# Kernel tuning notes

Measured on AMD Instinct MI355X. Metric: run time of the kernel, lower is better.

Reference implementation:

```python
import jax, jax.numpy as jnp
import numpy as np
from jax import lax

B = 512
THRESHOLD = 0.5
CFG = [64, 64, 'M', 128, 128, 'M', 256, 256, 256, 'M', 512, 512, 512, 'M', 512, 512, 512, 'M']  # VGG16


def _conv_relu(x, w, b):
    # x: [B,C,H,W], w: [O,I,3,3] (torch OIHW layout), pad=1 stride=1
    y = lax.conv_general_dilated(x, w, (1, 1), 'SAME',
                                 dimension_numbers=('NCHW', 'OIHW', 'NCHW'))
    return jax.nn.relu(y + b[None, :, None, None])


def _maxpool2(x):
    return lax.reduce_window(x, -jnp.inf, lax.max, (1, 1, 2, 2), (1, 1, 2, 2), 'VALID')


def _features(x, ws, bs):
    i = 0
    for c in CFG:
        if c == 'M':
            x = _maxpool2(x)
        else:
            x = _conv_relu(x, ws[i], bs[i])
            i += 1
    return x  # [B,512,1,1]


def _gcn(distance):
    # Faithful translation, including the source bug: 'onetensor' is zeros_like,
    # so mask==0 everywhere and A_hat collapses to the identity.
    n = distance.shape[0]
    zero = jnp.zeros_like(distance)
    one = jnp.zeros_like(distance)  # bug in original: torch.zeros_like for onetensor
    adj = jnp.where(distance > THRESHOLD, distance, zero)
    mask = jnp.where(distance > THRESHOLD, one, zero)
    idx = lax.top_k(adj, 10)[1]                                   # [n,10]
    top10 = jnp.zeros_like(adj).at[jnp.arange(n)[:, None], idx].set(1.0)
    top10 = top10 * mask
    a_hat = top10 + jnp.eye(n, dtype=distance.dtype)
    d_inv = jnp.diag(1.0 / jnp.sum(a_hat, axis=1))
    return lax.stop_gradient(a_hat @ d_inv)                        # [n,n]


def _forward(x, target, conv_ws, conv_bs, lin1_w, lin1_b, lin2_w, lin2_b, cls_w, cls_b):
    feat = _features(x, conv_ws, conv_bs).reshape(x.shape[0], -1)  # [B,512]
    h = jax.nn.relu(feat @ lin1_w + lin1_b)                        # [B,256]
    low = h @ lin2_w + lin2_b                                      # [B,128]
    graph_pre = jax.nn.sigmoid(low @ low.T)                        # [B,B]
    graph_gt = (target[:, None] == target[None, :]).astype(jnp.float32)
    mat = _gcn(graph_pre)                                          # [B,B], detached
    out = (mat @ feat) @ cls_w + cls_b                             # [B,10]
    return out, graph_pre, graph_gt


def setup_inputs() -> dict:
    key = jax.random.key(0)
    ks = iter(jax.random.split(key, 64))
    inp = {}
    inp['x'] = jax.random.normal(next(ks), (B, 3, 32, 32), dtype=jnp.float32)
    inp['target'] = jax.random.randint(next(ks), (B,), 0, 10)
    in_c, i = 3, 0
    for c in CFG:
        if c == 'M':
            continue
        scale = 1.0 / np.sqrt(in_c * 9.0)
        inp['conv%d_w' % i] = jax.random.normal(next(ks), (c, in_c, 3, 3), dtype=jnp.float32) * scale
        inp['conv%d_b' % i] = jnp.zeros((c,), dtype=jnp.float32)
        in_c, i = c, i + 1
    inp['lin1_w'] = jax.random.normal(next(ks), (512, 256), dtype=jnp.float32) * (1.0 / np.sqrt(512.0))
    inp['lin1_b'] = jnp.zeros((256,), dtype=jnp.float32)
    inp['lin2_w'] = jax.random.normal(next(ks), (256, 128), dtype=jnp.float32) * (1.0 / np.sqrt(256.0))
    inp['lin2_b'] = jnp.zeros((128,), dtype=jnp.float32)
    inp['cls_w'] = jax.random.normal(next(ks), (512, 10), dtype=jnp.float32) * (1.0 / np.sqrt(512.0))
    inp['cls_b'] = jnp.zeros((10,), dtype=jnp.float32)
    return inp


def reference(x, target,
              conv0_w, conv0_b, conv1_w, conv1_b, conv2_w, conv2_b, conv3_w, conv3_b,
              conv4_w, conv4_b, conv5_w, conv5_b, conv6_w, conv6_b, conv7_w, conv7_b,
              conv8_w, conv8_b, conv9_w, conv9_b, conv10_w, conv10_b, conv11_w, conv11_b,
              conv12_w, conv12_b,
              lin1_w, lin1_b, lin2_w, lin2_b, cls_w, cls_b):
    ws = [conv0_w, conv1_w, conv2_w, conv3_w, conv4_w, conv5_w, conv6_w,
          conv7_w, conv8_w, conv9_w, conv10_w, conv11_w, conv12_w]
    bs = [conv0_b, conv1_b, conv2_b, conv3_b, conv4_b, conv5_b, conv6_b,
          conv7_b, conv8_b, conv9_b, conv10_b, conv11_b, conv12_b]
    return _forward(x, target, ws, bs, lin1_w, lin1_b, lin2_w, lin2_b, cls_w, cls_b)
```

## Files before the change

kernel.cpp:

```cpp
#include <hip/hip_runtime.h>

typedef unsigned short u16;
typedef __bf16 bf16x8 __attribute__((ext_vector_type(8)));
typedef float floatx4 __attribute__((ext_vector_type(4)));

__device__ inline u16 f2bf(float f) {
    return __builtin_bit_cast(u16, (__bf16)f);
}
__device__ inline float bf2f(u16 h) {
    return __uint_as_float(((unsigned int)h) << 16);
}

__device__ __forceinline__ void async_copy16(u16* lds, const u16* g) {
    __builtin_amdgcn_global_load_lds(
        (const __attribute__((address_space(1))) unsigned int*)(uintptr_t)g,
        (__attribute__((address_space(3))) unsigned int*)(unsigned int)(uintptr_t)lds,
        16, 0, 0);
}

__global__ void zero_halo(u16* __restrict__ buf, int Hp, int C, int total8)
{
    int i = blockIdx.x * 256 + threadIdx.x;
    if (i >= total8) return;
    int c8 = i % (C / 8);
    int p  = i / (C / 8);
    int ring = 4 * Hp - 4;
    int h = p % ring;
    int b = p / ring;
    int y, x;
    if (h < Hp)              { y = 0;              x = h; }
    else if (h < 2 * Hp)     { y = Hp - 1;         x = h - Hp; }
    else if (h < 3 * Hp - 2) { y = h - 2 * Hp + 1; x = 0; }
    else                     { y = h - 3 * Hp + 3; x = Hp - 1; }
    uint4 z = make_uint4(0u, 0u, 0u, 0u);
    *(uint4*)(buf + ((size_t)((b * Hp + y) * Hp + x) * C) + c8 * 8) = z;
}

__global__ __launch_bounds__(256) void conv0_kernel(
    const float* __restrict__ x, const float* __restrict__ w,
    const float* __restrict__ bias, u16* __restrict__ out)
{
    __shared__ __align__(16) float xs[3][6][36];
    const int t  = threadIdx.x;
    const int b  = blockIdx.x >> 3;
    const int y0 = (blockIdx.x & 7) * 4;

    for (int i = t; i < 3 * 6 * 36; i += 256) {
        int ci  = i / 216;
        int rem = i % 216;
        int r   = rem / 36;
        int c   = rem % 36;
        int gy  = y0 - 1 + r;
        int gx  = c - 1;
        float v = 0.f;
        if ((unsigned)gy < 32u && (unsigned)gx < 32u)
            v = x[((b * 3 + ci) * 32 + gy) * 32 + gx];
        xs[ci][r][c] = v;
    }
    const int lane = t & 63;
    const int wv   = t >> 6;
    float wr[27];
    #pragma unroll
    for (int k = 0; k < 27; k++) wr[k] = w[lane * 27 + k];
    const float bz = bias[lane];
    __syncthreads();

    const int y = y0 + wv;
    u16* orow = out + ((size_t)((b * 34 + y + 1) * 34 + 1) * 64) + lane;
    for (int xg = 0; xg < 32; xg += 4) {
        float a0 = bz, a1 = bz, a2 = bz, a3 = bz;
        #pragma unroll
        for (int ci = 0; ci < 3; ci++) {
            #pragma unroll
            for (int rr = 0; rr < 3; rr++) {
                const float* row = &xs[ci][wv + rr][0];
                float4 c03 = *(const float4*)(row + xg);
                float2 c45 = *(const float2*)(row + xg + 4);
                float w0 = wr[ci * 9 + rr * 3 + 0];
                float w1 = wr[ci * 9 + rr * 3 + 1];
                float w2 = wr[ci * 9 + rr * 3 + 2];
                a0 += c03.x * w0 + c03.y * w1 + c03.z * w2;
                a1 += c03.y * w0 + c03.z * w1 + c03.w * w2;
                a2 += c03.z * w0 + c03.w * w1 + c45.x * w2;
                a3 += c03.w * w0 + c45.x * w1 + c45.y * w2;
            }
        }
        orow[(xg + 0) * 64] = f2bf(fmaxf(a0, 0.f));
        orow[(xg + 1) * 64] = f2bf(fmaxf(a1, 0.f));
        orow[(xg + 2) * 64] = f2bf(fmaxf(a2, 0.f));
        orow[(xg + 3) * 64] = f2bf(fmaxf(a3, 0.f));
    }
}

struct RepackArgs {
    const float* src[14];
    u16* dst[14];
    int p1[14];
    int p2[14];
    int startBlk[15];
    int nseg;
};

__global__ __launch_bounds__(256) void repack_all(RepackArgs a)
{
    __shared__ __align__(16) u16 lds[9216];
    int blk = blockIdx.x;
    int s = 0;
    #pragma unroll 1
    while (s + 1 < a.nseg && blk >= a.startBlk[s + 1]) s++;
    const int cb = blk - a.startBlk[s];
    const int t  = threadIdx.x;

    if (a.p2[s] == 0) {
        const int Cin = a.p1[s];
        const int logCin = __builtin_ctz(Cin);
        const float* src = a.src[s] + (size_t)cb * 9216;
        u16* dst = a.dst[s] + (size_t)cb * 9216;
        #pragma unroll
        for (int it = 0; it < 9; it++) {
            int j4 = it * 256 + t;
            float4 v = *(const float4*)(src + j4 * 4);
            ushort4 h;
            h.x = f2bf(v.x); h.y = f2bf(v.y); h.z = f2bf(v.z); h.w = f2bf(v.w);
            *(ushort4*)(lds + j4 * 4) = h;
        }
        __syncthreads();
        #pragma unroll
        for (int it = 0; it < 9; it++) {
            int o4   = (it * 256 + t) * 4;
            int ci   = o4 & (Cin - 1);
            int rest = o4 >> logCin;
            int co   = rest / 9;
            int sh   = rest - co * 9;
            int sb   = (co << logCin) * 9 + ci * 9 + sh;
            ushort4 h;
            h.x = lds[sb]; h.y = lds[sb + 9]; h.z = lds[sb + 18]; h.w = lds[sb + 27];
            *(ushort4*)(dst + o4) = h;
        }
    } else {
        const int K = a.p1[s], N = a.p2[s];
        const int ntx = N >> 6;
        const int k0 = (cb / ntx) * 64, n0 = (cb % ntx) * 64;
        const float* src = a.src[s];
        u16* dst = a.dst[s];
        const int r = t >> 4, c4 = (t & 15) * 4;
        #pragma unroll
        for (int rr = 0; rr < 64; rr += 16) {
            float4 v = *(const float4*)(src + (size_t)(k0 + r + rr) * N + n0 + c4);
            u16* p = lds + (r + rr) * 72 + c4;
            p[0] = f2bf(v.x); p[1] = f2bf(v.y); p[2] = f2bf(v.z); p[3] = f2bf(v.w);
        }
        __syncthreads();
        #pragma unroll
        for (int it = 0; it < 2; it++) {
            int ov = it * 256 + t;
            int n  = ov >> 3;
            int kq = (ov & 7) * 8;
            __align__(16) u16 h[8];
            #pragma unroll
            for (int j = 0; j < 8; j++) h[j] = lds[(kq + j) * 72 + n];
            *(uint4*)(dst + (size_t)(n0 + n) * K + k0 + kq) = *(uint4*)h;
        }
    }
}

template <int BM, int BN>
__global__ __launch_bounds__(256) void conv_gemm(
    const u16* __restrict__ in, const u16* __restrict__ wt,
    const float* __restrict__ bias, u16* __restrict__ out,
    float* __restrict__ partial, size_t pstride,
    int H, int Cin, int Cout, int logHW, int logW, int splitN,
    int outPad, int poolMode)
{
    constexpr int BK = 64;
    constexpr int WC = (BM == 256) ? BN : (BN / 2);
    constexpr int NT = WC / 16;
    constexpr int NB_A = BM / 32;
    constexpr int NB_B = BN / 32;
    constexpr int ASZ = BM * BK;
    constexpr int BSZ = BN * BK;
    __shared__ u16 As[2 * ASZ];
    __shared__ u16 Bs[2 * BSZ];

    const int Nblocks = Cout / BN;
    const int per = gridDim.x >> 3;
    const int bid = (blockIdx.x & 7) * per + (blockIdx.x >> 3);
    const int sp   = bid % splitN;
    const int tile = bid / splitN;
    const int m0 = (tile / Nblocks) * BM;
    const int n0 = (tile % Nblocks) * BN;

    const int t    = threadIdx.x;
    const int lane = t & 63;
    const int wave = t >> 6;
    const int quad = lane >> 4;
    const int l16  = lane & 15;
    const int wm   = (BM == 256) ? wave : (wave >> 1);
    const int wn   = (BM == 256) ? 0 : (wave & 1);
    const int W    = H;
    const int Wp   = H + 2;
    const int HW   = 1 << logHW;
    const int col8 = t & 7;
    const int r0   = t >> 3;
    const int scol = col8 ^ (r0 & 7);

    const int CinB = Cin * 2;

    int vA[NB_A];
    #pragma unroll
    for (int j = 0; j < NB_A; j++) {
        int m  = m0 + r0 + 32 * j;
        int b  = m >> logHW;
        int rm = m & (HW - 1);
        int y  = rm >> logW;
        int xx = rm & (W - 1);
        vA[j] = ((b * Wp + y + 1) * Wp + xx + 1) * CinB + scol * 16;
    }
    int vB[NB_B];
    #pragma unroll
    for (int j = 0; j < NB_B; j++)
        vB[j] = (n0 + r0 + 32 * j) * 9 * CinB + scol * 16;

    const int logKB = (Cin == 64) ? 0 : (Cin == 128) ? 1 : (Cin == 256) ? 2 : 3;
    const int KB  = 1 << logKB;
    const int T   = 9 * KB;
    const int len = T / splitN;
    const int it0 = sp * len;

    int s0 = it0 >> logKB;
    int c3 = s0 - (s0 / 3) * 3;
    int ta = ((s0 / 3 - 1) * Wp + (c3 - 1)) * CinB;
    int kb = (it0 & (KB - 1)) * 128;
    int tb = it0 * 128;

    const char* const inB = (const char*)in;
    const char* const wtB = (const char*)wt;

    floatx4 acc[4][NT];
    #pragma unroll
    for (int i = 0; i < 4; i++)
        #pragma unroll
        for (int j = 0; j < NT; j++)
            acc[i][j] = (floatx4){0.f, 0.f, 0.f, 0.f};

    const int sw = (l16 & 7) * 8;

    auto stage = [&](int ua, int tbv, int buf) {
        u16* la = As + buf * ASZ + t * 8;
        u16* lb = Bs + buf * BSZ + t * 8;
        #pragma unroll
        for (int j = 0; j < NB_A; j++)
            async_copy16(la + j * 2048, (const u16*)(inB + (ua + vA[j])));
        #pragma unroll
        for (int j = 0; j < NB_B; j++)
            async_copy16(lb + j * 2048, (const u16*)(wtB + (tbv + vB[j])));
    };
    auto advance = [&]() {
        tb += 128;
        kb += 128;
        if (kb == CinB) {
            kb = 0;
            ta += (c3 == 2) ? (Wp - 2) * CinB : CinB;
            c3 = (c3 == 2) ? 0 : c3 + 1;
        }
    };

    stage(ta + kb, tb, 0);
    advance();
    __syncthreads();

    int cur = 0;
    for (int it = 0; it < len; it++) {
        if (it + 1 < len) {
            stage(ta + kb, tb, cur ^ 1);
            advance();
        }
        const u16* Ab = As + cur * ASZ;
        const u16* Bb = Bs + cur * BSZ;
        #pragma unroll
        for (int kk = 0; kk < BK; kk += 32) {
            bf16x8 af[4], bfv[NT];
            int cbo = kk + quad * 8;
            #pragma unroll
            for (int mt = 0; mt < 4; mt++)
                af[mt] = *(const bf16x8*)(Ab + (wm * 64 + mt * 16 + l16) * 64 + (cbo ^ sw));
            #pragma unroll
            for (int nt = 0; nt < NT; nt++)
                bfv[nt] = *(const bf16x8*)(Bb + (wn * WC + nt * 16 + l16) * 64 + (cbo ^ sw));
            #pragma unroll
            for (int mt = 0; mt < 4; mt++)
                #pragma unroll
                for (int nt = 0; nt < NT; nt++)
                    acc[mt][nt] = __builtin_amdgcn_mfma_f32_16x16x32_bf16(
                        af[mt], bfv[nt], acc[mt][nt], 0, 0, 0);
        }
        __syncthreads();
        cur ^= 1;
    }

    const int ngb = n0 + wn * WC + l16;

    if (splitN > 1) {
        float* pout = partial + (size_t)sp * pstride;
        #pragma unroll
        for (int mt = 0; mt < 4; mt++)
            #pragma unroll
            for (int r = 0; r < 4; r++) {
                int mg = m0 + wm * 64 + mt * 16 + quad * 4 + r;
                float* op = pout + (size_t)mg * Cout + ngb;
                #pragma unroll
                for (int nt = 0; nt < NT; nt++)
                    op[nt * 16] = acc[mt][nt][r];
            }
        return;
    }

    float bzv[NT];
    #pragma unroll
    for (int nt = 0; nt < NT; nt++) bzv[nt] = bias[ngb + nt * 16];

    if (poolMode) {
        const int Hpo = (H >> 1) + 2;
        if (logW == 5) {
            #pragma unroll
            for (int mt = 0; mt < 2; mt++)
                #pragma unroll
                for (int rp = 0; rp < 2; rp++) {
                    int m1 = m0 + wm * 64 + mt * 16 + quad * 4 + 2 * rp;
                    int b  = m1 >> logHW;
                    int rm = m1 & (HW - 1);
                    int yp = (rm >> logW) >> 1;
                    int xp = (rm & (W - 1)) >> 1;
                    u16* op = out + (size_t)((b * Hpo + yp + 1) * Hpo + xp + 1) * Cout + ngb;
                    #pragma unroll
                    for (int nt = 0; nt < NT; nt++) {
                        float v = fmaxf(
                            fmaxf(acc[mt][nt][2 * rp], acc[mt][nt][2 * rp + 1]),
                            fmaxf(acc[mt + 2][nt][2 * rp], acc[mt + 2][nt][2 * rp + 1]));
                        op[nt * 16] = f2bf(fmaxf(v + bzv[nt], 0.f));
                    }
                }
        } else if (logW == 4) {
            #pragma unroll
            for (int mtp = 0; mtp < 2; mtp++)
                #pragma unroll
                for (int rp = 0; rp < 2; rp++) {
                    int mt = 2 * mtp;
                    int m1 = m0 + wm * 64 + mt * 16 + quad * 4 + 2 * rp;
                    int b  = m1 >> logHW;
                    int rm = m1 & (HW - 1);
                    int yp = (rm >> logW) >> 1;
                    int xp = (rm & (W - 1)) >> 1;
                    u16* op = out + (size_t)((b * Hpo + yp + 1) * Hpo + xp + 1) * Cout + ngb;
                    #pragma unroll
                    for (int nt = 0; nt < NT; nt++) {
                        float v = fmaxf(
                            fmaxf(acc[mt][nt][2 * rp], acc[mt][nt][2 * rp + 1]),
                            fmaxf(acc[mt + 1][nt][2 * rp], acc[mt + 1][nt][2 * rp + 1]));
                        op[nt * 16] = f2bf(fmaxf(v + bzv[nt], 0.f));
                    }
                }
        } else {
            #pragma unroll
            for (int mt = 0; mt < 4; mt++)
                #pragma unroll
                for (int rp = 0; rp < 2; rp++) {
                    int m1 = m0 + wm * 64 + mt * 16 + quad * 4 + 2 * rp;
                    int b  = m1 >> logHW;
                    int rm = m1 & (HW - 1);
                    int yp = (rm >> logW) >> 1;
                    int xp = (rm & (W - 1)) >> 1;
                    u16* op = out + (size_t)((b * Hpo + yp + 1) * Hpo + xp + 1) * Cout + ngb;
                    #pragma unroll
                    for (int nt = 0; nt < NT; nt++) {
                        float a = fmaxf(acc[mt][nt][2 * rp], acc[mt][nt][2 * rp + 1]);
                        float p = __shfl_xor(a, 32, 64);
                        float v = fmaxf(a, p);
                        if (quad < 2)
                            op[nt * 16] = f2bf(fmaxf(v + bzv[nt], 0.f));
                    }
                }
        }
        return;
    }

    #pragma unroll
    for (int mt = 0; mt < 4; mt++) {
        #pragma unroll
        for (int r = 0; r < 4; r++) {
            int mg = m0 + wm * 64 + mt * 16 + quad * 4 + r;
            size_t obase;
            if (outPad) {
                int b  = mg >> logHW;
                int rm = mg & (HW - 1);
                int y  = rm >> logW;
                int xx = rm & (W - 1);
                obase = (size_t)((b * Wp + y + 1) * Wp + xx + 1) * Cout;
            } else {
                obase = (size_t)mg * Cout;
            }
            u16* op = out + obase + ngb;
            #pragma unroll
            for (int nt = 0; nt < NT; nt++)
                op[nt * 16] = f2bf(fmaxf(acc[mt][nt][r] + bzv[nt], 0.f));
        }
    }
}

__global__ void reduce_split(const float* __restrict__ partial,
                             const float* __restrict__ bias, u16* __restrict__ out,
                             int MN, int C, int logC, int splitN, size_t pstride,
                             int H, int logHW, int logW, int outPad)
{
    int i4 = (blockIdx.x * 256 + threadIdx.x) * 4;
    if (i4 >= MN) return;
    float4 s = *(const float4*)(partial + i4);
    for (int sp = 1; sp < splitN; sp++) {
        float4 p = *(const float4*)(partial + (size_t)sp * pstride + i4);
        s.x += p.x; s.y += p.y; s.z += p.z; s.w += p.w;
    }
    int n = i4 & (C - 1);
    int m = i4 >> logC;
    size_t obase;
    if (outPad) {
        int Wp = H + 2;
        int b  = m >> logHW;
        int rm = m & ((1 << logHW) - 1);
        int y  = rm >> logW;
        int xx = rm & (H - 1);
        obase = (size_t)((b * Wp + y + 1) * Wp + xx + 1) * C;
    } else {
        obase = (size_t)m * C;
    }
    ushort4 o;
    o.x = f2bf(fmaxf(s.x + bias[n + 0], 0.f));
    o.y = f2bf(fmaxf(s.y + bias[n + 1], 0.f));
    o.z = f2bf(fmaxf(s.z + bias[n + 2], 0.f));
    o.w = f2bf(fmaxf(s.w + bias[n + 3], 0.f));
    *(ushort4*)(out + obase + n) = o;
}

__global__ void reduce_pool(const float* __restrict__ partial,
                            const float* __restrict__ bias, u16* __restrict__ out,
                            int total4, int C, int splitN, size_t pstride,
                            int H, int outPad)
{
    int idx = blockIdx.x * 256 + threadIdx.x;
    if (idx >= total4) return;
    int c4 = idx % (C / 4);
    int p  = idx / (C / 4);
    int Ho = H >> 1;
    int xp = p % Ho; p /= Ho;
    int yp = p % Ho;
    int b  = p / Ho;
    int n  = c4 * 4;
    float4 best;
    bool first = true;
    #pragma unroll
    for (int dy = 0; dy < 2; dy++)
        #pragma unroll
        for (int dx = 0; dx < 2; dx++) {
            int m = (b * H + 2 * yp + dy) * H + 2 * xp + dx;
            const float* q = partial + (size_t)m * C + n;
            float4 s = *(const float4*)q;
            for (int sp = 1; sp < splitN; sp++) {
                float4 pp = *(const float4*)(q + (size_t)sp * pstride);
                s.x += pp.x; s.y += pp.y; s.z += pp.z; s.w += pp.w;
            }
            if (first) { best = s; first = false; }
            else {
                best.x = fmaxf(best.x, s.x); best.y = fmaxf(best.y, s.y);
                best.z = fmaxf(best.z, s.z); best.w = fmaxf(best.w, s.w);
            }
        }
    size_t obase;
    if (outPad) {
        int Hpo = Ho + 2;
        obase = (size_t)((b * Hpo + yp + 1) * Hpo + xp + 1) * C;
    } else {
        obase = (size_t)((b * Ho + yp) * Ho + xp) * C;
    }
    ushort4 o;
    o.x = f2bf(fmaxf(best.x + bias[n + 0], 0.f));
    o.y = f2bf(fmaxf(best.y + bias[n + 1], 0.f));
    o.z = f2bf(fmaxf(best.z + bias[n + 2], 0.f));
    o.w = f2bf(fmaxf(best.w + bias[n + 3], 0.f));
    *(ushort4*)(out + obase + n) = o;
}

template <bool RELU, bool OUTBF>
__global__ __launch_bounds__(256) void gemm64(
    const u16* __restrict__ A, const u16* __restrict__ Bt,
    const float* __restrict__ bias, void* __restrict__ outv,
    int M, int N, int K)
{
    constexpr int LDP = 72;
    __shared__ u16 As[64 * LDP];
    __shared__ u16 Bs[64 * LDP];

    const int nb = N >> 6;
    const int m0 = (blockIdx.x / nb) * 64;
    const int n0 = (blockIdx.x % nb) * 64;
    const int t = threadIdx.x, lane = t & 63, wave = t >> 6;
    const int quad = lane >> 4, l16 = lane & 15;
    const int wm = wave >> 1, wn = wave & 1;
    const int col8 = t & 7, r0 = t >> 3;

    floatx4 acc[2][2];
    #pragma unroll
    for (int i = 0; i < 2; i++)
        #pragma unroll
        for (int j = 0; j < 2; j++)
            acc[i][j] = (floatx4){0.f, 0.f, 0.f, 0.f};

    for (int kb = 0; kb < K; kb += 64) {
        #pragma unroll
        for (int j = 0; j < 2; j++) {
            int row = r0 + 32 * j;
            *(uint4*)(As + row * LDP + col8 * 8) =
                *(const uint4*)(A + (size_t)(m0 + row) * K + kb + col8 * 8);
            *(uint4*)(Bs + row * LDP + col8 * 8) =
                *(const uint4*)(Bt + (size_t)(n0 + row) * K + kb + col8 * 8);
        }
        __syncthreads();
        #pragma unroll
        for (int kk = 0; kk < 64; kk += 32) {
            bf16x8 af[2], bfv[2];
            #pragma unroll
            for (int mt = 0; mt < 2; mt++)
                af[mt] = *(const bf16x8*)(As + (wm * 32 + mt * 16 + l16) * LDP + kk + quad * 8);
            #pragma unroll
            for (int nt = 0; nt < 2; nt++)
                bfv[nt] = *(const bf16x8*)(Bs + (wn * 32 + nt * 16 + l16) * LDP + kk + quad * 8);
            #pragma unroll
            for (int mt = 0; mt < 2; mt++)
                #pragma unroll
                for (int nt = 0; nt < 2; nt++)
                    acc[mt][nt] = __builtin_amdgcn_mfma_f32_16x16x32_bf16(
                        af[mt], bfv[nt], acc[mt][nt], 0, 0, 0);
        }
        __syncthreads();
    }
    #pragma unroll
    for (int mt = 0; mt < 2; mt++) {
        #pragma unroll
        for (int nt = 0; nt < 2; nt++) {
            #pragma unroll
            for (int r = 0; r < 4; r++) {
                int mg = m0 + wm * 32 + mt * 16 + quad * 4 + r;
                int ng = n0 + wn * 32 + nt * 16 + l16;
                float v = acc[mt][nt][r] + bias[ng];
                if (RELU) v = fmaxf(v, 0.f);
                if (OUTBF) ((u16*)outv)[(size_t)mg * N + ng] = f2bf(v);
                else       ((float*)outv)[(size_t)mg * N + ng] = v;
            }
        }
    }
}

__global__ __launch_bounds__(256) void graph_tile(
    const float* __restrict__ low, const int* __restrict__ target,
    float* __restrict__ gpre, float* __restrict__ ggt)
{
    __shared__ float Al[64 * 132];
    __shared__ float Bl[128 * 68];
    const int t = threadIdx.x;
    const int gr0 = (blockIdx.x >> 3) * 64;
    const int gc0 = (blockIdx.x & 7) * 64;

    #pragma unroll
    for (int j = 0; j < 32; j++) {
        int flat = t + 256 * j;
        int k = flat & 127;
        int rc = flat >> 7;
        Al[rc * 132 + k] = low[(size_t)(gr0 + rc) * 128 + k];
        Bl[k * 68 + rc]  = low[(size_t)(gc0 + rc) * 128 + k];
    }
    __syncthreads();

    const int tx = t & 15, ty = t >> 4;
    float acc[4][4];
    #pragma unroll
    for (int r = 0; r < 4; r++)
        #pragma unroll
        for (int c = 0; c < 4; c++) acc[r][c] = 0.f;

    for (int k = 0; k < 128; k++) {
        float a[4], b[4];
        #pragma unroll
        for (int r = 0; r < 4; r++) a[r] = Al[(ty * 4 + r) * 132 + k];
        #pragma unroll
        for (int c = 0; c < 4; c++) b[c] = Bl[k * 68 + tx * 4 + c];
        #pragma unroll
        for (int r = 0; r < 4; r++)
            #pragma unroll
            for (int c = 0; c < 4; c++) acc[r][c] += a[r] * b[c];
    }
    #pragma unroll
    for (int r = 0; r < 4; r++) {
        int row = gr0 + ty * 4 + r;
        int tr  = target[row];
        float4 gp, gg;
        float* pp = (float*)&gp;
        float* gg_ = (float*)&gg;
        #pragma unroll
        for (int c = 0; c < 4; c++) {
            pp[c]  = 1.f / (1.f + __expf(-acc[r][c]));
            gg_[c] = (tr == target[gc0 + tx * 4 + c]) ? 1.f : 0.f;
        }
        *(float4*)(gpre + (size_t)row * 512 + gc0 + tx * 4) = gp;
        *(float4*)(ggt  + (size_t)row * 512 + gc0 + tx * 4) = gg;
    }
}

__global__ __launch_bounds__(256) void cls_kernel(
    const u16* __restrict__ feat, const float* __restrict__ w,
    const float* __restrict__ bias, float* __restrict__ out)
{
    __shared__ float ws[5120];
    const int t = threadIdx.x;
    for (int i = t; i < 5120; i += 256) ws[i] = w[i];
    __syncthreads();
    const int lane = t & 63;
    const int row  = blockIdx.x * 4 + (t >> 6);
    float a[10];
    #pragma unroll
    for (int j = 0; j < 10; j++) a[j] = 0.f;
    #pragma unroll
    for (int i = 0; i < 8; i++) {
        int k = i * 64 + lane;
        float f = bf2f(feat[(size_t)row * 512 + k]);
        #pragma unroll
        for (int j = 0; j < 10; j++) a[j] += f * ws[k * 10 + j];
    }
    #pragma unroll
    for (int j = 0; j < 10; j++)
        #pragma unroll
        for (int off = 32; off > 0; off >>= 1)
            a[j] += __shfl_down(a[j], off, 64);
    if (lane == 0) {
        #pragma unroll
        for (int j = 0; j < 10; j++) out[row * 10 + j] = a[j] + bias[j];
    }
}

extern "C" void kernel_launch(void* const* d_in, const int* in_sizes, int n_in,
                              void* d_out, int out_size, void* d_ws, size_t ws_size,
                              hipStream_t stream)
{
    const float* x      = (const float*)d_in[0];
    const int*   target = (const int*)d_in[1];
    const float* conv_w[13];
    const float* conv_b[13];
    for (int i = 0; i < 13; i++) {
        conv_w[i] = (const float*)d_in[2 + 2 * i];
        conv_b[i] = (const float*)d_in[3 + 2 * i];
    }
    const float* lin1_w = (const float*)d_in[28];
    const float* lin1_b = (const float*)d_in[29];
    const float* lin2_w = (const float*)d_in[30];
    const float* lin2_b = (const float*)d_in[31];
    const float* cls_w  = (const float*)d_in[32];
    const float* cls_b  = (const float*)d_in[33];
    float* out = (float*)d_out;

    static const int cin_arr[13]  = {3, 64, 64, 128, 128, 256, 256, 256, 512, 512, 512, 512, 512};
    static const int cout_arr[13] = {64, 64, 128, 128, 256, 256, 256, 512, 512, 512, 512, 512, 512};

    char* ws = (char*)d_ws;
    size_t off = 0;
    const size_t R0SZ = (size_t)512 * 34 * 34 * 64 * 2;
    const size_t R1SZ = (size_t)512 * 34 * 34 * 64 * 2;
    char* R0raw = ws + off; off += R0SZ;
    char* R1raw = ws + off; off += R1SZ;
    u16* R0 = (u16*)R0raw;
    u16* R1 = (u16*)R1raw;
    float* PA = (float*)(R0raw + 20971520);
    float* PB = (float*)(R1raw + 20971520);
    u16* wt[13];
    for (int i = 1; i < 13; i++) {
        wt[i] = (u16*)(ws + off);
        off += (size_t)cout_arr[i] * 9 * cin_arr[i] * 2;
    }
    u16* wtl1 = (u16*)(ws + off); off += (size_t)256 * 512 * 2;
    u16* wtl2 = (u16*)(ws + off); off += (size_t)128 * 256 * 2;
    u16* hbuf = (u16*)(ws + off); off += (size_t)512 * 256 * 2;
    float* lowbuf = (float*)(ws + off); off += (size_t)512 * 128 * 4;

    RepackArgs ra;
    int nb = 0, blk = 0;
    ra.startBlk[0] = 0;
    for (int i = 1; i < 13; i++) {
        ra.src[nb] = conv_w[i];
        ra.dst[nb] = wt[i];
        ra.p1[nb] = cin_arr[i];
        ra.p2[nb] = 0;
        blk += cout_arr[i] * cin_arr[i] / 1024;
        nb++; ra.startBlk[nb] = blk;
    }
    ra.src[nb] = lin1_w; ra.dst[nb] = wtl1; ra.p1[nb] = 512; ra.p2[nb] = 256;
    blk += (512 / 64) * (256 / 64);
    nb++; ra.startBlk[nb] = blk;
    ra.src[nb] = lin2_w; ra.dst[nb] = wtl2; ra.p1[nb] = 256; ra.p2[nb] = 128;
    blk += (256 / 64) * (128 / 64);
    nb++; ra.startBlk[nb] = blk;
    ra.nseg = nb;
    repack_all<<<blk, 256, 0, stream>>>(ra);

    auto zh = [&](u16* buf, int Hp, int C) {
        int total8 = 512 * (4 * Hp - 4) * (C / 8);
        zero_halo<<<(total8 + 255) / 256, 256, 0, stream>>>(buf, Hp, C, total8);
    };
    auto launch_conv = [&](int li, int Hl, int bm, int bn, u16* inb, u16* outb,
                           float* part, int splitN, int outPad, int poolMode) {
        int Cin = cin_arr[li], Cout = cout_arr[li];
        int M = 512 * Hl * Hl;
        int logW = __builtin_ctz(Hl);
        int logHW = 2 * logW;
        size_t pstride = (size_t)M * Cout;
        int grid = (M / bm) * (Cout / bn) * splitN;
        if (bm == 256) {
            conv_gemm<256, 64><<<grid, 256, 0, stream>>>(
                inb, wt[li], conv_b[li], outb, part, pstride,
                Hl, Cin, Cout, logHW, logW, splitN, outPad, poolMode);
        } else if (bn == 128) {
            conv_gemm<128, 128><<<grid, 256, 0, stream>>>(
                inb, wt[li], conv_b[li], outb, part, pstride,
                Hl, Cin, Cout, logHW, logW, splitN, outPad, poolMode);
        } else {
            conv_gemm<128, 64><<<grid, 256, 0, stream>>>(
                inb, wt[li], conv_b[li], outb, part, pstride,
                Hl, Cin, Cout, logHW, logW, splitN, outPad, poolMode);
        }
    };
    auto launch_reduce = [&](int li, int Hl, u16* outb, float* part, int splitN, int outPad) {
        int Cout = cout_arr[li];
        int M = 512 * Hl * Hl;
        int logW = __builtin_ctz(Hl);
        size_t pstride = (size_t)M * Cout;
        int MN = M * Cout;
        reduce_split<<<(MN / 4 + 255) / 256, 256, 0, stream>>>(
            part, conv_b[li], outb, MN, Cout, __builtin_ctz(Cout),
            splitN, pstride, Hl, 2 * logW, logW, outPad);
    };
    auto launch_reduce_pool = [&](int li, int Hl, u16* outb, float* part, int splitN, int outPad) {
        int Cout = cout_arr[li];
        int M = 512 * Hl * Hl;
        size_t pstride = (size_t)M * Cout;
        int total4 = 512 * (Hl / 2) * (Hl / 2) * Cout / 4;
        reduce_pool<<<(total4 + 255) / 256, 256, 0, stream>>>(
            part, conv_b[li], outb, total4, Cout, splitN, pstride, Hl, outPad);
    };

    zh(R0, 34, 64);
    conv0_kernel<<<512 * 8, 256, 0, stream>>>(x, conv_w[0], conv_b[0], R0);

    zh(R1, 18, 64);
    launch_conv(1, 32, 256, 64, R0, R1, nullptr, 1, 0, 1);
    zh(R0, 18, 128);
    launch_conv(2, 16, 128, 128, R1, R0, nullptr, 1, 1, 0);
    zh(R1, 10, 128);
    launch_conv(3, 16, 128, 128, R0, R1, nullptr, 1, 0, 1);
    zh(R0, 10, 256);
    launch_conv(4, 8, 128, 128, R1, R0, nullptr, 1, 1, 0);
    zh(R1, 10, 256);
    launch_conv(5, 8, 128, 128, R0, R1, nullptr, 1, 1, 0);
    zh(R0, 6, 256);
    launch_conv(6, 8, 128, 128, R1, R0, nullptr, 1, 0, 1);
    zh(R1, 6, 512);
    launch_conv(7, 4, 128, 128, R0, R1, PB, 2, 1, 0);
    launch_reduce(7, 4, R1, PB, 2, 1);
    zh(R0, 6, 512);
    launch_conv(8, 4, 128, 128, R1, R0, PA, 2, 1, 0);
    launch_reduce(8, 4, R0, PA, 2, 1);
    zh(R1, 4, 512);
    launch_conv(9, 4, 128, 128, R0, R1, PB, 2, 0, 0);
    launch_reduce_pool(9, 4, R1, PB, 2, 1);
    zh(R0, 4, 512);
    launch_conv(10, 2, 128, 64, R1, R0, PA, 4, 1, 0);
    launch_reduce(10, 2, R0, PA, 4, 1);
    zh(R1, 4, 512);
    launch_conv(11, 2, 128, 64, R0, R1, PB, 4, 1, 0);
    launch_reduce(11, 2, R1, PB, 4, 1);
    launch_conv(12, 2, 128, 64, R1, R0, PA, 4, 0, 0);
    launch_reduce_pool(12, 2, R0, PA, 4, 0);

    u16* feat = R0;
    gemm64<true, true><<<(512 / 64) * (256 / 64), 256, 0, stream>>>(
        feat, wtl1, lin1_b, hbuf, 512, 256, 512);
    gemm64<false, false><<<(512 / 64) * (128 / 64), 256, 0, stream>>>(
        hbuf, wtl2, lin2_b, lowbuf, 512, 128, 256);
    graph_tile<<<64, 256, 0, stream>>>(lowbuf, target, out + 5120, out + 5120 + 262144);
    cls_kernel<<<128, 256, 0, stream>>>(feat, cls_w, cls_b, out);
}
```

Baseline: 698.9 us.

## Load conv A operand directly from global into registers, skipping LDS staging

The activation (A) tile of the implicit-GEMM conv is no longer staged through shared memory. Each lane now reads its MFMA fragments straight from global memory, and only the weight tile keeps the double-buffered LDS path. Launch bounds are raised to 8 blocks per CU to exploit the smaller LDS footprint. The trade-off is that A data is no longer shared across the waves in a block, so there is more redundant global and L2 traffic. The global loads are also not prefetched ahead of use, so their latency is exposed to the MFMA loop.

```diff
diff --git a/kernel.cpp b/kernel.cpp
--- a/kernel.cpp
+++ b/kernel.cpp
@@ -165,7 +165,7 @@
 }
 
 template <int BM, int BN>
-__global__ __launch_bounds__(256) void conv_gemm(
+__global__ __launch_bounds__(256, 8) void conv_gemm(
     const u16* __restrict__ in, const u16* __restrict__ wt,
     const float* __restrict__ bias, u16* __restrict__ out,
     float* __restrict__ partial, size_t pstride,
@@ -175,11 +175,8 @@
     constexpr int BK = 64;
     constexpr int WC = (BM == 256) ? BN : (BN / 2);
     constexpr int NT = WC / 16;
-    constexpr int NB_A = BM / 32;
     constexpr int NB_B = BN / 32;
-    constexpr int ASZ = BM * BK;
     constexpr int BSZ = BN * BK;
-    __shared__ u16 As[2 * ASZ];
     __shared__ u16 Bs[2 * BSZ];
 
     const int Nblocks = Cout / BN;
@@ -206,15 +203,15 @@
 
     const int CinB = Cin * 2;
 
-    int vA[NB_A];
-    #pragma unroll
-    for (int j = 0; j < NB_A; j++) {
-        int m  = m0 + r0 + 32 * j;
+    int aBase[4];
+    #pragma unroll
+    for (int mt = 0; mt < 4; mt++) {
+        int m  = m0 + wm * 64 + mt * 16 + l16;
         int b  = m >> logHW;
         int rm = m & (HW - 1);
         int y  = rm >> logW;
         int xx = rm & (W - 1);
-        vA[j] = ((b * Wp + y + 1) * Wp + xx + 1) * CinB + scol * 16;
+        aBase[mt] = ((b * Wp + y + 1) * Wp + xx + 1) * CinB + quad * 16;
     }
     int vB[NB_B];
     #pragma unroll
@@ -245,45 +242,43 @@
 
     const int sw = (l16 & 7) * 8;
 
-    auto stage = [&](int ua, int tbv, int buf) {
-        u16* la = As + buf * ASZ + t * 8;
+    auto stageB = [&](int tbv, int buf) {
         u16* lb = Bs + buf * BSZ + t * 8;
-        #pragma unroll
-        for (int j = 0; j < NB_A; j++)
-            async_copy16(la + j * 2048, (const u16*)(inB + (ua + vA[j])));
         #pragma unroll
         for (int j = 0; j < NB_B; j++)
             async_copy16(lb + j * 2048, (const u16*)(wtB + (tbv + vB[j])));
     };
-    auto advance = [&]() {
-        tb += 128;
+
+    stageB(tb, 0);
+    tb += 128;
+    __syncthreads();
+
+    int cur = 0;
+    for (int it = 0; it < len; it++) {
+        if (it + 1 < len) {
+            stageB(tb, cur ^ 1);
+            tb += 128;
+        }
+        const int offs = ta + kb;
         kb += 128;
         if (kb == CinB) {
             kb = 0;
             ta += (c3 == 2) ? (Wp - 2) * CinB : CinB;
             c3 = (c3 == 2) ? 0 : c3 + 1;
         }
-    };
-
-    stage(ta + kb, tb, 0);
-    advance();
-    __syncthreads();
-
-    int cur = 0;
-    for (int it = 0; it < len; it++) {
-        if (it + 1 < len) {
-            stage(ta + kb, tb, cur ^ 1);
-            advance();
-        }
-        const u16* Ab = As + cur * ASZ;
+
+        bf16x8 af[2][4];
+        #pragma unroll
+        for (int kk2 = 0; kk2 < 2; kk2++)
+            #pragma unroll
+            for (int mt = 0; mt < 4; mt++)
+                af[kk2][mt] = *(const bf16x8*)(inB + (offs + aBase[mt] + kk2 * 64));
+
         const u16* Bb = Bs + cur * BSZ;
         #pragma unroll
-        for (int kk = 0; kk < BK; kk += 32) {
-            bf16x8 af[4], bfv[NT];
-            int cbo = kk + quad * 8;
-            #pragma unroll
-            for (int mt = 0; mt < 4; mt++)
-                af[mt] = *(const bf16x8*)(Ab + (wm * 64 + mt * 16 + l16) * 64 + (cbo ^ sw));
+        for (int kk2 = 0; kk2 < 2; kk2++) {
+            int cbo = kk2 * 32 + quad * 8;
+            bf16x8 bfv[NT];
             #pragma unroll
             for (int nt = 0; nt < NT; nt++)
                 bfv[nt] = *(const bf16x8*)(Bb + (wn * WC + nt * 16 + l16) * 64 + (cbo ^ sw));
@@ -292,7 +287,7 @@
                 #pragma unroll
                 for (int nt = 0; nt < NT; nt++)
                     acc[mt][nt] = __builtin_amdgcn_mfma_f32_16x16x32_bf16(
-                        af[mt], bfv[nt], acc[mt][nt], 0, 0, 0);
+                        af[kk2][mt], bfv[nt], acc[mt][nt], 0, 0, 0);
         }
         __syncthreads();
         cur ^= 1;
```

After: 1.589 ms. +127.4%, slower.

## Add halo-tiled implicit-GEMM conv kernel staging input patch once in LDS

Applied to the files above, without the earlier changes.

Adds a conv_halo kernel that loads the padded input rows for a block's output tile (plus halo) into LDS once, then reads all nine 3x3 taps from that shared patch instead of re-staging the A operand per tap. Only the weight tiles are double-buffered through LDS across the K loop. Layers 1-3 switch to this kernel, which cuts redundant global and LDS traffic for the activation operand. The cost is a large LDS allocation per block that may lower occupancy, and the input layout assumptions are hardcoded as template parameters.

```diff
diff --git a/kernel.cpp b/kernel.cpp
--- a/kernel.cpp
+++ b/kernel.cpp
@@ -396,6 +396,217 @@
                 int y  = rm >> logW;
                 int xx = rm & (W - 1);
                 obase = (size_t)((b * Wp + y + 1) * Wp + xx + 1) * Cout;
+            } else {
+                obase = (size_t)mg * Cout;
+            }
+            u16* op = out + obase + ngb;
+            #pragma unroll
+            for (int nt = 0; nt < NT; nt++)
+                op[nt * 16] = f2bf(fmaxf(acc[mt][nt][r] + bzv[nt], 0.f));
+        }
+    }
+}
+
+template <int BM, int BN, int W, int CIN>
+__global__ __launch_bounds__(256) void conv_halo(
+    const u16* __restrict__ in, const u16* __restrict__ wt,
+    const float* __restrict__ bias, u16* __restrict__ out,
+    int outPad, int poolMode)
+{
+    constexpr int BK = 64;
+    constexpr int WC = (BM == 256) ? BN : (BN / 2);
+    constexpr int NT = WC / 16;
+    constexpr int NB_B = BN / 32;
+    constexpr int BSZ = BN * BK;
+    constexpr int Wp = W + 2;
+    constexpr int R  = BM / W;
+    constexpr int P  = (R + 2) * Wp;
+    constexpr int CinB = CIN * 2;
+    constexpr int CH = CinB / 16;
+    constexpr int LOG_CH = (CH == 8) ? 3 : 4;
+    constexpr int HALO_CHUNKS = P * CH;
+    constexpr int ROUNDS = (HALO_CHUNKS + 255) / 256;
+    constexpr int logW = (W == 32) ? 5 : 4;
+    constexpr int logHW = 2 * logW;
+    constexpr int HW = 1 << logHW;
+    constexpr int KB = CIN / 64;
+    constexpr int T  = 9 * KB;
+
+    __shared__ __align__(16) u16 Ah[P * CH * 8];
+    __shared__ __align__(16) u16 Bs[2 * BSZ];
+
+    constexpr int Nblocks = 1;
+    static_assert(true, "");
+    const int per = gridDim.x >> 3;
+    const int bid = (blockIdx.x & 7) * per + (blockIdx.x >> 3);
+    const int m0 = (bid / Nblocks) * BM;
+    const int n0 = (bid % Nblocks) * BN;
+
+    const int t    = threadIdx.x;
+    const int lane = t & 63;
+    const int wave = t >> 6;
+    const int quad = lane >> 4;
+    const int l16  = lane & 15;
+    const int wm   = (BM == 256) ? wave : (wave >> 1);
+    const int wn   = (BM == 256) ? 0 : (wave & 1);
+    const int col8 = t & 7;
+    const int r0   = t >> 3;
+    const int scol = col8 ^ (r0 & 7);
+
+    const int b  = m0 >> logHW;
+    const int y0 = (m0 & (HW - 1)) >> logW;
+
+    const char* hsrc = (const char*)in + (size_t)((b * Wp + y0) * Wp) * CinB;
+    #pragma unroll
+    for (int rd = 0; rd < ROUNDS; rd++) {
+        int i = rd * 256 + t;
+        if ((HALO_CHUNKS % 256 == 0) || i < HALO_CHUNKS) {
+            int pp   = i >> LOG_CH;
+            int si   = i ^ (pp & 7);
+            async_copy16(Ah + i * 8, (const u16*)(hsrc + (size_t)si * 16));
+        }
+    }
+
+    int vB[NB_B];
+    #pragma unroll
+    for (int j = 0; j < NB_B; j++)
+        vB[j] = (n0 + r0 + 32 * j) * 9 * CinB + scol * 16;
+    const char* const wtB = (const char*)wt;
+    auto stageB = [&](int tbv, int buf) {
+        u16* lb = Bs + buf * BSZ + t * 8;
+        #pragma unroll
+        for (int j = 0; j < NB_B; j++)
+            async_copy16(lb + j * 2048, (const u16*)(wtB + (tbv + vB[j])));
+    };
+
+    int pBase[4];
+    #pragma unroll
+    for (int mt = 0; mt < 4; mt++) {
+        int dm = wm * 64 + mt * 16 + l16;
+        pBase[mt] = (dm >> logW) * Wp + (dm & (W - 1));
+    }
+
+    floatx4 acc[4][NT];
+    #pragma unroll
+    for (int i = 0; i < 4; i++)
+        #pragma unroll
+        for (int j = 0; j < NT; j++)
+            acc[i][j] = (floatx4){0.f, 0.f, 0.f, 0.f};
+
+    const int sw = (l16 & 7) * 8;
+    const char* const AhB = (const char*)Ah;
+
+    stageB(0, 0);
+    __syncthreads();
+
+    int cur = 0, tb = 128;
+    int pOff = 0, c3 = 0, cb = 0;
+    for (int it = 0; it < T; it++) {
+        if (it + 1 < T) { stageB(tb, cur ^ 1); tb += 128; }
+        const int pO = pOff, cbv = cb;
+        cb += 128;
+        if (cb == CinB) {
+            cb = 0;
+            pOff += (c3 == 2) ? (Wp - 2) : 1;
+            c3 = (c3 == 2) ? 0 : c3 + 1;
+        }
+
+        bf16x8 af[2][4];
+        #pragma unroll
+        for (int mt = 0; mt < 4; mt++) {
+            int p  = pBase[mt] + pO;
+            int pc = p & 7;
+            int ab = p * CinB + cbv;
+            #pragma unroll
+            for (int kk2 = 0; kk2 < 2; kk2++) {
+                int kq = kk2 * 4 + quad;
+                af[kk2][mt] = *(const bf16x8*)(AhB + ab + ((kq ^ pc) << 4));
+            }
+        }
+
+        const u16* Bb = Bs + cur * BSZ;
+        #pragma unroll
+        for (int kk2 = 0; kk2 < 2; kk2++) {
+            int cbo = kk2 * 32 + quad * 8;
+            bf16x8 bfv[NT];
+            #pragma unroll
+            for (int nt = 0; nt < NT; nt++)
+                bfv[nt] = *(const bf16x8*)(Bb + (wn * WC + nt * 16 + l16) * 64 + (cbo ^ sw));
+            #pragma unroll
+            for (int mt = 0; mt < 4; mt++)
+                #pragma unroll
+                for (int nt = 0; nt < NT; nt++)
+                    acc[mt][nt] = __builtin_amdgcn_mfma_f32_16x16x32_bf16(
+                        af[kk2][mt], bfv[nt], acc[mt][nt], 0, 0, 0);
+        }
+        __syncthreads();
+        cur ^= 1;
+    }
+
+    const int ngb = n0 + wn * WC + l16;
+    float bzv[NT];
+    #pragma unroll
+    for (int nt = 0; nt < NT; nt++) bzv[nt] = bias[ngb + nt * 16];
+    const int Cout = BN;
+    const int H = W;
+
+    if (poolMode) {
+        const int Hpo = (H >> 1) + 2;
+        if (logW == 5) {
+            #pragma unroll
+            for (int mt = 0; mt < 2; mt++)
+                #pragma unroll
+                for (int rp = 0; rp < 2; rp++) {
+                    int m1 = m0 + wm * 64 + mt * 16 + quad * 4 + 2 * rp;
+                    int bb = m1 >> logHW;
+                    int rm = m1 & (HW - 1);
+                    int yp = (rm >> logW) >> 1;
+                    int xp = (rm & (W - 1)) >> 1;
+                    u16* op = out + (size_t)((bb * Hpo + yp + 1) * Hpo + xp + 1) * Cout + ngb;
+                    #pragma unroll
+                    for (int nt = 0; nt < NT; nt++) {
+                        float v = fmaxf(
+                            fmaxf(acc[mt][nt][2 * rp], acc[mt][nt][2 * rp + 1]),
+                            fmaxf(acc[mt + 2][nt][2 * rp], acc[mt + 2][nt][2 * rp + 1]));
+                        op[nt * 16] = f2bf(fmaxf(v + bzv[nt], 0.f));
+                    }
+                }
+        } else {
+            #pragma unroll
+            for (int mtp = 0; mtp < 2; mtp++)
+                #pragma unroll
+                for (int rp = 0; rp < 2; rp++) {
+                    int mt = 2 * mtp;
+                    int m1 = m0 + wm * 64 + mt * 16 + quad * 4 + 2 * rp;
+                    int bb = m1 >> logHW;
+                    int rm = m1 & (HW - 1);
+                    int yp = (rm >> logW) >> 1;
+                    int xp = (rm & (W - 1)) >> 1;
+                    u16* op = out + (size_t)((bb * Hpo + yp + 1) * Hpo + xp + 1) * Cout + ngb;
+                    #pragma unroll
+                    for (int nt = 0; nt < NT; nt++) {
+                        float v = fmaxf(
+                            fmaxf(acc[mt][nt][2 * rp], acc[mt][nt][2 * rp + 1]),
+                            fmaxf(acc[mt + 1][nt][2 * rp], acc[mt + 1][nt][2 * rp + 1]));
+                        op[nt * 16] = f2bf(fmaxf(v + bzv[nt], 0.f));
+                    }
+                }
+        }
+        return;
+    }
+
+    #pragma unroll
+    for (int mt = 0; mt < 4; mt++) {
+        #pragma unroll
+        for (int r = 0; r < 4; r++) {
+            int mg = m0 + wm * 64 + mt * 16 + quad * 4 + r;
+            size_t obase;
+            if (outPad) {
+                int bb = mg >> logHW;
+                int rm = mg & (HW - 1);
+                int y  = rm >> logW;
+                int xx = rm & (W - 1);
+                obase = (size_t)((bb * Wp + y + 1) * Wp + xx + 1) * Cout;
             } else {
                 obase = (size_t)mg * Cout;
             }
@@ -756,11 +967,14 @@
     conv0_kernel<<<512 * 8, 256, 0, stream>>>(x, conv_w[0], conv_b[0], R0);
 
     zh(R1, 18, 64);
-    launch_conv(1, 32, 256, 64, R0, R1, nullptr, 1, 0, 1);
+    conv_halo<256, 64, 32, 64><<<2048, 256, 0, stream>>>(
+        R0, wt[1], conv_b[1], R1, 0, 1);
     zh(R0, 18, 128);
-    launch_conv(2, 16, 128, 128, R1, R0, nullptr, 1, 1, 0);
+    conv_halo<128, 128, 16, 64><<<1024, 256, 0, stream>>>(
+        R1, wt[2], conv_b[2], R0, 1, 0);
     zh(R1, 10, 128);
-    launch_conv(3, 16, 128, 128, R0, R1, nullptr, 1, 0, 1);
+    conv_halo<128, 128, 16, 128><<<1024, 256, 0, stream>>>(
+        R0, wt[3], conv_b[3], R1, 0, 1);
     zh(R0, 10, 256);
     launch_conv(4, 8, 128, 128, R1, R0, nullptr, 1, 1, 0);
     zh(R1, 10, 256);
```

Measured after the change: 683.1 us. 2.3% less time.
